# Performance work log

Measured on AMD Instinct MI355X. Metric: run time of the kernel, lower is better.

The kernel has to match this reference:

```python
import jax, jax.numpy as jnp
import numpy as np

WS = 7       # window size per spatial dim
SHIFT = 3    # cyclic shift = WS // 2
HEADS = 6


def _rel_pos_index():
    # [N, N] index into the (2*WS-1)^3 relative-position-bias table
    c = np.stack(np.meshgrid(np.arange(WS), np.arange(WS), np.arange(WS), indexing='ij')).reshape(3, -1)
    rel = (c[:, :, None] - c[:, None, :]).transpose(1, 2, 0) + (WS - 1)
    rel[:, :, 0] *= (2 * WS - 1) ** 2
    rel[:, :, 1] *= (2 * WS - 1)
    return rel.sum(-1)


def _attn_mask(D, H, W):
    # shifted-window attention mask: [nW, N, N] with 0 / -100
    img = np.zeros((D, H, W))
    sl = (slice(0, -WS), slice(-WS, -SHIFT), slice(-SHIFT, None))
    cnt = 0
    for d in sl:
        for h in sl:
            for w in sl:
                img[d, h, w] = cnt
                cnt += 1
    m = img.reshape(D // WS, WS, H // WS, WS, W // WS, WS).transpose(0, 2, 4, 1, 3, 5).reshape(-1, WS ** 3)
    return np.where(m[:, None, :] != m[:, :, None], -100.0, 0.0).astype(np.float32)


def _ln(x, g, b):
    mu = x.mean(-1, keepdims=True)
    var = ((x - mu) ** 2).mean(-1, keepdims=True)
    return (x - mu) * jax.lax.rsqrt(var + 1e-5) * g + b


def _win_part(x):
    B, D, H, W, C = x.shape
    x = x.reshape(B, D // WS, WS, H // WS, WS, W // WS, WS, C)
    return x.transpose(0, 1, 3, 5, 2, 4, 6, 7).reshape(B, -1, WS ** 3, C)


def _win_rev(xw, D, H, W):
    B, _, _, C = xw.shape
    x = xw.reshape(B, D // WS, H // WS, W // WS, WS, WS, WS, C)
    return x.transpose(0, 1, 4, 2, 5, 3, 6, 7).reshape(B, D, H, W, C)


def setup_inputs() -> dict:
    key = jax.random.key(0)
    ks = jax.random.split(key, 8)
    C, dff, Nh = 192, 768, HEADS
    s = 0.02
    return {
        'x': jax.random.normal(ks[0], (2, 28, 28, 28, C), jnp.float32),
        'ln1_g': jnp.ones((C,), jnp.float32),
        'ln1_b': jnp.zeros((C,), jnp.float32),
        'qkv_w': jax.random.normal(ks[1], (3 * C, C), jnp.float32) * s,
        'qkv_b': jnp.zeros((3 * C,), jnp.float32),
        'rpb': jax.random.normal(ks[2], ((2 * WS - 1) ** 3, Nh), jnp.float32) * s,
        'proj_w': jax.random.normal(ks[3], (C, C), jnp.float32) * s,
        'proj_b': jnp.zeros((C,), jnp.float32),
        'ln2_g': jnp.ones((C,), jnp.float32),
        'ln2_b': jnp.zeros((C,), jnp.float32),
        'fc1_w': jax.random.normal(ks[4], (dff, C), jnp.float32) * s,
        'fc1_b': jnp.zeros((dff,), jnp.float32),
        'fc2_w': jax.random.normal(ks[5], (C, dff), jnp.float32) * s,
        'fc2_b': jnp.zeros((C,), jnp.float32),
    }


def reference(x, ln1_g, ln1_b, qkv_w, qkv_b, rpb, proj_w, proj_b, ln2_g, ln2_b, fc1_w, fc1_b, fc2_w, fc2_b):
    B, D, H, W, C = x.shape
    hd = C // HEADS
    N = WS ** 3
    idx = jnp.asarray(_rel_pos_index())          # [N, N] int
    mask = jnp.asarray(_attn_mask(D, H, W))      # [nW, N, N]

    shortcut = x
    h = _ln(x, ln1_g, ln1_b)
    h = jnp.roll(h, (-SHIFT, -SHIFT, -SHIFT), axis=(1, 2, 3))
    xw = _win_part(h)                            # [B, nW, N, C]
    nW = xw.shape[1]

    qkv = xw @ qkv_w.T + qkv_b                   # [B, nW, N, 3C]
    qkv = qkv.reshape(B, nW, N, 3, HEADS, hd).transpose(3, 0, 1, 4, 2, 5)  # [3,B,nW,h,N,hd]
    q, k, v = qkv[0], qkv[1], qkv[2]

    scale = hd ** -0.5
    attn = jnp.einsum('bwhnd,bwhmd->bwhnm', q * scale, k)  # [B,nW,h,N,N]
    bias = rpb[idx].transpose(2, 0, 1)           # [h, N, N]
    attn = attn + bias + mask[None, :, None]
    attn = jax.nn.softmax(attn, axis=-1)

    o = jnp.einsum('bwhnm,bwhmd->bwhnd', attn, v)
    o = o.transpose(0, 1, 3, 2, 4).reshape(B, nW, N, C)
    o = o @ proj_w.T + proj_b
    o = _win_rev(o, D, H, W)
    o = jnp.roll(o, (SHIFT, SHIFT, SHIFT), axis=(1, 2, 3))

    x = shortcut + o
    h2 = _ln(x, ln2_g, ln2_b)
    h2 = jax.nn.gelu(h2 @ fc1_w.T + fc1_b, approximate=False)
    return x + (h2 @ fc2_w.T + fc2_b)
```

## Files before the change

### kernel.cpp

```cpp
#include <hip/hip_runtime.h>
#include <hip/hip_bf16.h>
#include <math.h>

typedef __hip_bfloat16 bf16;
typedef unsigned short u16;
typedef __attribute__((ext_vector_type(8))) short bf16x8;
typedef __attribute__((ext_vector_type(4))) float f32x4;
typedef __attribute__((ext_vector_type(16))) float f32x16;
typedef __attribute__((ext_vector_type(4))) unsigned u32x4;

__device__ __forceinline__ float us2f(u16 u) { return __uint_as_float(((unsigned)u) << 16); }
__device__ __forceinline__ u16 f2us(float f) { bf16 h = __float2bfloat16(f); return *(u16*)&h; }

__device__ __forceinline__ float wave_bcast_sum(float v) {
#pragma unroll
    for (int off = 32; off > 0; off >>= 1) v += __shfl_down(v, off);
    return __shfl(v, 0);
}

__device__ __forceinline__ void glds16(const u16* g, u16* l) {
    __builtin_amdgcn_global_load_lds((const __attribute__((address_space(1))) void*)g,
                                     (__attribute__((address_space(3))) void*)l, 16, 0, 0);
}

__global__ __launch_bounds__(256) void k_f2b(const float* __restrict__ in, u16* __restrict__ out, int n) {
    int i = blockIdx.x * 256 + threadIdx.x;
    if (i < n) out[i] = f2us(in[i]);
}

__global__ __launch_bounds__(256) void k_bias(const float* __restrict__ rpb, float* __restrict__ bt) {
    int idx = blockIdx.x * 256 + threadIdx.x;
    if (idx >= 6 * 352 * 352) return;
    int h = idx / (352 * 352);
    int r = idx - h * (352 * 352);
    int m = r / 352, n = r - m * 352;
    float v = 0.0f;
    if (m < 343 && n < 343) {
        int ni = n / 49, nr = n - ni * 49, nj = nr / 7, nk = nr - nj * 7;
        int mi = m / 49, mr = m - mi * 49, mj = mr / 7, mk = mr - mj * 7;
        int d = (ni - mi) * 169 + (nj - mj) * 13 + (nk - mk) + 1098;
        v = rpb[d * 6 + h] * 1.4426950408889634f;
    }
    bt[idx] = v;
}

__global__ __launch_bounds__(256) void k_ln1_winpart(
    const float* __restrict__ x, const float* __restrict__ g, const float* __restrict__ b,
    u16* __restrict__ out)
{
    int lane = threadIdx.x & 63;
    int t = blockIdx.x * 4 + (threadIdx.x >> 6);
    int bidx = t / (64 * 343);
    int r = t - bidx * (64 * 343);
    int w = r / 343;
    int n = r - w * 343;
    int wd = w >> 4, wh = (w >> 2) & 3, ww = w & 3;
    int i = n / 49, rem = n - i * 49;
    int j = rem / 7, k = rem - j * 7;
    int sd = wd * 7 + i + 3; if (sd >= 28) sd -= 28;
    int sh = wh * 7 + j + 3; if (sh >= 28) sh -= 28;
    int sw = ww * 7 + k + 3; if (sw >= 28) sw -= 28;
    size_t src = ((((size_t)bidx * 28 + sd) * 28 + sh) * 28 + sw) * 192;
    float v0 = x[src + lane], v1 = x[src + lane + 64], v2 = x[src + lane + 128];
    float s  = wave_bcast_sum(v0 + v1 + v2);
    float mu = s * (1.0f / 192.0f);
    float s2 = wave_bcast_sum(v0 * v0 + v1 * v1 + v2 * v2);
    float rs = rsqrtf(s2 * (1.0f / 192.0f) - mu * mu + 1e-5f);
    u16* op = out + (size_t)t * 192;
    op[lane]       = f2us((v0 - mu) * rs * g[lane]       + b[lane]);
    op[lane + 64]  = f2us((v1 - mu) * rs * g[lane + 64]  + b[lane + 64]);
    op[lane + 128] = f2us((v2 - mu) * rs * g[lane + 128] + b[lane + 128]);
}

__global__ __launch_bounds__(256) void k_add_winrev_ln2(
    const float* __restrict__ x, const u16* __restrict__ projw,
    const float* __restrict__ g, const float* __restrict__ b,
    float* __restrict__ x1, u16* __restrict__ h2)
{
    int lane = threadIdx.x & 63;
    int t = blockIdx.x * 4 + (threadIdx.x >> 6);
    int sw_ = t % 28, t1 = t / 28;
    int sh_ = t1 % 28, t2 = t1 / 28;
    int sd_ = t2 % 28, bidx = t2 / 28;
    int rd = sd_ + 25; if (rd >= 28) rd -= 28;
    int rh = sh_ + 25; if (rh >= 28) rh -= 28;
    int rw = sw_ + 25; if (rw >= 28) rw -= 28;
    int wd = rd / 7, i = rd - wd * 7;
    int wh = rh / 7, j = rh - wh * 7;
    int ww = rw / 7, k = rw - ww * 7;
    int w = (wd << 4) + (wh << 2) + ww;
    int n = (i * 7 + j) * 7 + k;
    size_t src = (((size_t)(bidx * 64 + w)) * 343 + n) * 192;
    const float* xp = x + (size_t)t * 192;
    float v0 = xp[lane]       + us2f(projw[src + lane]);
    float v1 = xp[lane + 64]  + us2f(projw[src + lane + 64]);
    float v2 = xp[lane + 128] + us2f(projw[src + lane + 128]);
    float* op = x1 + (size_t)t * 192;
    op[lane] = v0; op[lane + 64] = v1; op[lane + 128] = v2;
    float s  = wave_bcast_sum(v0 + v1 + v2);
    float mu = s * (1.0f / 192.0f);
    float s2 = wave_bcast_sum(v0 * v0 + v1 * v1 + v2 * v2);
    float rs = rsqrtf(s2 * (1.0f / 192.0f) - mu * mu + 1e-5f);
    u16* hp = h2 + (size_t)t * 192;
    hp[lane]       = f2us((v0 - mu) * rs * g[lane]       + b[lane]);
    hp[lane + 64]  = f2us((v1 - mu) * rs * g[lane + 64]  + b[lane + 64]);
    hp[lane + 128] = f2us((v2 - mu) * rs * g[lane + 128] + b[lane + 128]);
}

template<int ACT, int OUT>
__global__ __launch_bounds__(256) void k_gemm_mfma(
    const u16* __restrict__ A, const u16* __restrict__ W, const float* __restrict__ bias,
    u16* __restrict__ outB, float* __restrict__ outF, const float* __restrict__ resid,
    int M, int Nc, int K)
{
    __shared__ __align__(16) u16 As[2][128 * 32];
    __shared__ __align__(16) u16 Bs[2][64 * 32];
    int tid = threadIdx.x;
    int lane = tid & 63, wv = tid >> 6;
    int quad = lane >> 4, l16 = lane & 15;
    int m0 = blockIdx.y << 7, n0 = blockIdx.x << 6;

    f32x4 acc[2][4] = {};
    int rowA0 = tid >> 2;
    int rowA1 = rowA0 + 64;
    int koff = (tid & 3) << 3;

    const u16* gA0 = A + (size_t)(m0 + rowA0) * K + koff;
    const u16* gA1 = A + (size_t)(m0 + rowA1) * K + koff;
    const u16* gB0 = W + (size_t)(n0 + rowA0) * K + koff;

    int nt = K >> 5;
    glds16(gA0, &As[0][wv * 512]);
    glds16(gA1, &As[0][2048 + wv * 512]);
    glds16(gB0, &Bs[0][wv * 512]);
    asm volatile("s_waitcnt vmcnt(0)" ::: "memory");
    __builtin_amdgcn_s_barrier();

    int cur = 0;
    for (int t = 0; t < nt; ++t) {
        if (t + 1 < nt) {
            int k1 = (t + 1) << 5;
            glds16(gA0 + k1, &As[cur ^ 1][wv * 512]);
            glds16(gA1 + k1, &As[cur ^ 1][2048 + wv * 512]);
            glds16(gB0 + k1, &Bs[cur ^ 1][wv * 512]);
        }
        bf16x8 af[2], bfr[4];
#pragma unroll
        for (int mt = 0; mt < 2; mt++)
            af[mt] = *(const bf16x8*)&As[cur][(wv * 32 + mt * 16 + l16) * 32 + quad * 8];
#pragma unroll
        for (int nt2 = 0; nt2 < 4; nt2++)
            bfr[nt2] = *(const bf16x8*)&Bs[cur][(nt2 * 16 + l16) * 32 + quad * 8];
#pragma unroll
        for (int mt = 0; mt < 2; mt++)
#pragma unroll
            for (int nt2 = 0; nt2 < 4; nt2++)
                acc[mt][nt2] = __builtin_amdgcn_mfma_f32_16x16x32_bf16(af[mt], bfr[nt2], acc[mt][nt2], 0, 0, 0);
        asm volatile("s_waitcnt vmcnt(0)" ::: "memory");
        __builtin_amdgcn_s_barrier();
        cur ^= 1;
    }
#pragma unroll
    for (int mt = 0; mt < 2; mt++) {
#pragma unroll
        for (int nt2 = 0; nt2 < 4; nt2++) {
#pragma unroll
            for (int r = 0; r < 4; r++) {
                int m = m0 + wv * 32 + mt * 16 + quad * 4 + r;
                int n = n0 + nt2 * 16 + l16;
                float v = acc[mt][nt2][r] + bias[n];
                if (ACT == 1) v = 0.5f * v * (1.0f + erff(v * 0.70710678118654752f));
                size_t off = (size_t)m * Nc + n;
                if (OUT == 1) outB[off] = f2us(v);
                else outF[off] = resid[off] + v;
            }
        }
    }
}

__global__ __launch_bounds__(256) void k_attn(
    const u16* __restrict__ qkv, const float* __restrict__ biasT, u16* __restrict__ o_win)
{
    int head = blockIdx.x;
    int w = blockIdx.y;
    int bidx = blockIdx.z;
    __shared__ __align__(16) u16 Ks[352 * 40];
    __shared__ __align__(16) u16 Vt[32 * 360];
    __shared__ float invs[4][32];
    __shared__ unsigned char lab[352];
    int tid = threadIdx.x;
    int lane = tid & 63, wv = tid >> 6;
    int hi = lane >> 5, l31 = lane & 31;
    size_t base = ((size_t)(bidx * 64 + w)) * 343;

    for (int i = tid; i < 2816; i += 256) {
        int m = i >> 3;
        int d4 = (i & 7) << 2;
        ushort4 kv = {0, 0, 0, 0}, vv = {0, 0, 0, 0};
        if (m < 343) {
            size_t off = (base + m) * 576 + head * 32 + d4;
            kv = *(const ushort4*)(qkv + off + 192);
            vv = *(const ushort4*)(qkv + off + 384);
        }
        *(ushort4*)&Ks[m * 40 + d4] = kv;
        Vt[(d4 + 0) * 360 + m] = vv.x;
        Vt[(d4 + 1) * 360 + m] = vv.y;
        Vt[(d4 + 2) * 360 + m] = vv.z;
        Vt[(d4 + 3) * 360 + m] = vv.w;
    }
    int wd = w >> 4, wh = (w >> 2) & 3, ww = w & 3;
    for (int n = tid; n < 352; n += 256) {
        unsigned char lv = 255;
        if (n < 343) {
            int i = n / 49, rem = n - i * 49;
            int j = rem / 7, k = rem - j * 7;
            int gd = wd * 7 + i, gh = wh * 7 + j, gw = ww * 7 + k;
            int ld_ = (gd < 21) ? 0 : ((gd < 25) ? 1 : 2);
            int lh_ = (gh < 21) ? 0 : ((gh < 25) ? 1 : 2);
            int lw_ = (gw < 21) ? 0 : ((gw < 25) ? 1 : 2);
            lv = (unsigned char)(ld_ * 9 + lh_ * 3 + lw_);
        }
        lab[n] = lv;
    }
    __syncthreads();

    const float SL = 0.17677669529663687f * 1.4426950408889634f;
    const f32x16 z16 = {0,0,0,0,0,0,0,0,0,0,0,0,0,0,0,0};

    for (int tile = wv; tile < 11; tile += 4) {
        int n0 = tile * 32;
        int nq = n0 + l31; if (nq > 342) nq = 342;
        const u16* qp = qkv + (base + nq) * 576 + head * 32;
        bf16x8 bq0 = *(const bf16x8*)(qp + hi * 8);
        bf16x8 bq1 = *(const bf16x8*)(qp + 16 + hi * 8);
        unsigned lr = lab[n0 + l31];
        const float* bq = biasT + (size_t)head * 352 * 352 + n0 + l31;

        f32x16 o = z16;
        float psum = 0.0f;
        for (int c = 0; c < 11; ++c) {
            int mb = c * 32;
            const u16* kp = &Ks[(mb + l31) * 40 + hi * 8];
            bf16x8 ka0 = *(const bf16x8*)kp;
            bf16x8 ka1 = *(const bf16x8*)(kp + 16);
            f32x16 s = __builtin_amdgcn_mfma_f32_32x32x16_bf16(ka0, bq0, z16, 0, 0, 0);
            s = __builtin_amdgcn_mfma_f32_32x32x16_bf16(ka1, bq1, s, 0, 0, 0);
            unsigned labw[4];
#pragma unroll
            for (int g = 0; g < 4; ++g)
                labw[g] = *(const unsigned*)&lab[mb + hi * 4 + g * 8];
            float p[16];
#pragma unroll
            for (int r = 0; r < 16; ++r) {
                int g = r >> 2, q = r & 3;
                float bb = bq[(size_t)(mb + 4 * hi + 8 * g + q) * 352];
                float e = exp2f(fmaf(s[r], SL, bb));
                p[r] = (((labw[g] >> (8 * q)) & 255u) == lr) ? e : 0.0f;
                psum += p[r];
            }
            unsigned pk0 = (unsigned)f2us(p[0])  | ((unsigned)f2us(p[1])  << 16);
            unsigned pk1 = (unsigned)f2us(p[2])  | ((unsigned)f2us(p[3])  << 16);
            unsigned pk2 = (unsigned)f2us(p[4])  | ((unsigned)f2us(p[5])  << 16);
            unsigned pk3 = (unsigned)f2us(p[6])  | ((unsigned)f2us(p[7])  << 16);
            unsigned pk4 = (unsigned)f2us(p[8])  | ((unsigned)f2us(p[9])  << 16);
            unsigned pk5 = (unsigned)f2us(p[10]) | ((unsigned)f2us(p[11]) << 16);
            unsigned pk6 = (unsigned)f2us(p[12]) | ((unsigned)f2us(p[13]) << 16);
            unsigned pk7 = (unsigned)f2us(p[14]) | ((unsigned)f2us(p[15]) << 16);
            asm volatile("v_permlane32_swap_b32 %0, %1" : "+v"(pk0), "+v"(pk2));
            asm volatile("v_permlane32_swap_b32 %0, %1" : "+v"(pk1), "+v"(pk3));
            asm volatile("v_permlane32_swap_b32 %0, %1" : "+v"(pk4), "+v"(pk6));
            asm volatile("v_permlane32_swap_b32 %0, %1" : "+v"(pk5), "+v"(pk7));
            u32x4 A1 = {pk0, pk1, pk2, pk3};
            u32x4 A2 = {pk4, pk5, pk6, pk7};
            bf16x8 pa0 = __builtin_bit_cast(bf16x8, A1);
            bf16x8 pa1 = __builtin_bit_cast(bf16x8, A2);
            const u16* vp = &Vt[l31 * 360 + mb + hi * 8];
            bf16x8 vb0 = *(const bf16x8*)vp;
            bf16x8 vb1 = *(const bf16x8*)(vp + 16);
            o = __builtin_amdgcn_mfma_f32_32x32x16_bf16(pa0, vb0, o, 0, 0, 0);
            o = __builtin_amdgcn_mfma_f32_32x32x16_bf16(pa1, vb1, o, 0, 0, 0);
        }
        psum += __shfl_xor(psum, 32);
        float inv = 1.0f / psum;
        invs[wv][l31] = inv;
        asm volatile("s_waitcnt lgkmcnt(0)" ::: "memory");
        __builtin_amdgcn_sched_barrier(0);
#pragma unroll
        for (int r = 0; r < 16; ++r) {
            int crow = (r & 3) + 8 * (r >> 2) + 4 * hi;
            int n = n0 + crow;
            if (n < 343) {
                u16* op = o_win + (base + n) * 192 + head * 32;
                op[l31] = f2us(o[r] * invs[wv][crow]);
            }
        }
    }
}

extern "C" void kernel_launch(void* const* d_in, const int* in_sizes, int n_in,
                              void* d_out, int out_size, void* d_ws, size_t ws_size,
                              hipStream_t stream)
{
    const float* x      = (const float*)d_in[0];
    const float* ln1_g  = (const float*)d_in[1];
    const float* ln1_b  = (const float*)d_in[2];
    const float* qkv_w  = (const float*)d_in[3];
    const float* qkv_b  = (const float*)d_in[4];
    const float* rpb    = (const float*)d_in[5];
    const float* proj_w = (const float*)d_in[6];
    const float* proj_b = (const float*)d_in[7];
    const float* ln2_g  = (const float*)d_in[8];
    const float* ln2_b  = (const float*)d_in[9];
    const float* fc1_w  = (const float*)d_in[10];
    const float* fc1_b  = (const float*)d_in[11];
    const float* fc2_w  = (const float*)d_in[12];
    const float* fc2_b  = (const float*)d_in[13];

    const int M = 43904;
    const size_t MC  = (size_t)M * 192;
    const size_t MC2 = MC * 2;

    char* ws = (char*)d_ws;
    u16* hA     = (u16*)ws;
    u16* qkvb   = (u16*)(ws + MC2);
    u16* projw  = (u16*)(ws + MC2);
    u16* gbuf   = (u16*)(ws + MC2);
    u16* fc1_wb = (u16*)(ws + 51u * 1024 * 1024);
    u16* fc2_wb = (u16*)(ws + 51u * 1024 * 1024 + 294912);
    float* out  = (float*)d_out;
    u16* qkv_wb  = (u16*)d_out;
    u16* proj_wb = (u16*)d_out + 110592;
    float* biasT = (float*)((char*)d_out + 4u * 1024 * 1024);

    k_f2b<<<432, 256, 0, stream>>>(qkv_w, qkv_wb, 110592);
    k_f2b<<<144, 256, 0, stream>>>(proj_w, proj_wb, 36864);
    k_bias<<<2904, 256, 0, stream>>>(rpb, biasT);
    k_ln1_winpart<<<M / 4, 256, 0, stream>>>(x, ln1_g, ln1_b, hA);
    k_gemm_mfma<0, 1><<<dim3(9, 343), 256, 0, stream>>>(hA, qkv_wb, qkv_b, qkvb, nullptr, nullptr, M, 576, 192);
    k_attn<<<dim3(6, 64, 2), 256, 0, stream>>>(qkvb, biasT, hA);
    k_f2b<<<576, 256, 0, stream>>>(fc1_w, fc1_wb, 147456);
    k_f2b<<<576, 256, 0, stream>>>(fc2_w, fc2_wb, 147456);
    k_gemm_mfma<0, 1><<<dim3(3, 343), 256, 0, stream>>>(hA, proj_wb, proj_b, projw, nullptr, nullptr, M, 192, 192);
    k_add_winrev_ln2<<<M / 4, 256, 0, stream>>>(x, projw, ln2_g, ln2_b, out, hA);
    const int CH0 = 22016, CH1 = 21888;
    k_gemm_mfma<1, 1><<<dim3(12, 172), 256, 0, stream>>>(hA, fc1_wb, fc1_b, gbuf, nullptr, nullptr, CH0, 768, 192);
    k_gemm_mfma<0, 2><<<dim3(3, 172), 256, 0, stream>>>(gbuf, fc2_wb, fc2_b, nullptr, out, out, CH0, 192, 768);
    k_gemm_mfma<1, 1><<<dim3(12, 171), 256, 0, stream>>>(hA + (size_t)CH0 * 192, fc1_wb, fc1_b, gbuf, nullptr, nullptr, CH1, 768, 192);
    k_gemm_mfma<0, 2><<<dim3(3, 171), 256, 0, stream>>>(gbuf, fc2_wb, fc2_b, nullptr, out + (size_t)CH0 * 192, out + (size_t)CH0 * 192, CH1, 192, 768);
}
```

Before: 341.3 us.

## Widen GEMM K-tile with swizzled LDS, specialize unmasked attention windows, fuse prep kernels

The GEMM now stages 64-wide K tiles with an XOR-swizzled LDS layout, which halves the number of barrier iterations and is meant to reduce bank conflicts. In attention, the bias table is transposed so each lane reads it as contiguous float4 values that seed the MFMA accumulator. Windows that need no shift mask take a fast path that skips the label comparison. The small weight-conversion and bias-table kernels are merged into fewer launches. The larger LDS footprint may reduce GEMM occupancy.

```diff
diff --git a/kernel.cpp b/kernel.cpp
--- a/kernel.cpp
+++ b/kernel.cpp
@@ -23,25 +23,37 @@
                                      (__attribute__((address_space(3))) void*)l, 16, 0, 0);
 }
 
-__global__ __launch_bounds__(256) void k_f2b(const float* __restrict__ in, u16* __restrict__ out, int n) {
-    int i = blockIdx.x * 256 + threadIdx.x;
-    if (i < n) out[i] = f2us(in[i]);
-}
-
-__global__ __launch_bounds__(256) void k_bias(const float* __restrict__ rpb, float* __restrict__ bt) {
+__global__ __launch_bounds__(256) void k_prep(
+    const float* __restrict__ qkv_w, const float* __restrict__ proj_w,
+    const float* __restrict__ rpb,
+    u16* __restrict__ qkv_wb, u16* __restrict__ proj_wb, float* __restrict__ biasT)
+{
     int idx = blockIdx.x * 256 + threadIdx.x;
+    if (idx < 110592) { qkv_wb[idx] = f2us(qkv_w[idx]); return; }
+    idx -= 110592;
+    if (idx < 36864) { proj_wb[idx] = f2us(proj_w[idx]); return; }
+    idx -= 36864;
     if (idx >= 6 * 352 * 352) return;
     int h = idx / (352 * 352);
     int r = idx - h * (352 * 352);
-    int m = r / 352, n = r - m * 352;
+    int n = r / 352, m = r - n * 352;
     float v = 0.0f;
     if (m < 343 && n < 343) {
         int ni = n / 49, nr = n - ni * 49, nj = nr / 7, nk = nr - nj * 7;
         int mi = m / 49, mr = m - mi * 49, mj = mr / 7, mk = mr - mj * 7;
         int d = (ni - mi) * 169 + (nj - mj) * 13 + (nk - mk) + 1098;
-        v = rpb[d * 6 + h] * 1.4426950408889634f;
-    }
-    bt[idx] = v;
+        v = rpb[d * 6 + h] * 5.656854249492381f;
+    }
+    biasT[h * (352 * 352) + n * 352 + m] = v;
+}
+
+__global__ __launch_bounds__(256) void k_f2b2(
+    const float* __restrict__ fc1_w, const float* __restrict__ fc2_w,
+    u16* __restrict__ fc1_wb, u16* __restrict__ fc2_wb)
+{
+    int idx = blockIdx.x * 256 + threadIdx.x;
+    if (idx < 147456) fc1_wb[idx] = f2us(fc1_w[idx]);
+    else fc2_wb[idx - 147456] = f2us(fc2_w[idx - 147456]);
 }
 
 __global__ __launch_bounds__(256) void k_ln1_winpart(
@@ -113,62 +125,70 @@
     u16* __restrict__ outB, float* __restrict__ outF, const float* __restrict__ resid,
     int M, int Nc, int K)
 {
-    __shared__ __align__(16) u16 As[2][128 * 32];
-    __shared__ __align__(16) u16 Bs[2][64 * 32];
+    __shared__ __align__(16) u16 As[2][128 * 64];
+    __shared__ __align__(16) u16 Bs[2][64 * 64];
     int tid = threadIdx.x;
     int lane = tid & 63, wv = tid >> 6;
     int quad = lane >> 4, l16 = lane & 15;
     int m0 = blockIdx.y << 7, n0 = blockIdx.x << 6;
 
     f32x4 acc[2][4] = {};
-    int rowA0 = tid >> 2;
-    int rowA1 = rowA0 + 64;
-    int koff = (tid & 3) << 3;
-
-    const u16* gA0 = A + (size_t)(m0 + rowA0) * K + koff;
-    const u16* gA1 = A + (size_t)(m0 + rowA1) * K + koff;
-    const u16* gB0 = W + (size_t)(n0 + rowA0) * K + koff;
-
-    int nt = K >> 5;
-    glds16(gA0, &As[0][wv * 512]);
-    glds16(gA1, &As[0][2048 + wv * 512]);
-    glds16(gB0, &Bs[0][wv * 512]);
+
+    int srow = wv * 8 + (lane >> 3);
+    int swz  = ((lane & 7) << 3) ^ (((lane >> 3) & 7) << 3);
+    const u16* gA = A + (size_t)(m0 + srow) * K + swz;
+    const u16* gB = W + (size_t)(n0 + srow) * K + swz;
+    int rsA = 32 * K;
+
+    int nst = K >> 6;
+#define STAGE(buf, k0)                                                        \
+    {                                                                         \
+        _Pragma("unroll")                                                     \
+        for (int i = 0; i < 4; i++)                                           \
+            glds16(gA + (size_t)i * rsA + (k0), &As[buf][(i * 4 + wv) * 512]); \
+        _Pragma("unroll")                                                     \
+        for (int i = 0; i < 2; i++)                                           \
+            glds16(gB + (size_t)i * rsA + (k0), &Bs[buf][(i * 4 + wv) * 512]); \
+    }
+
+    STAGE(0, 0);
     asm volatile("s_waitcnt vmcnt(0)" ::: "memory");
     __builtin_amdgcn_s_barrier();
 
+    int rswz = (l16 & 7) << 3;
     int cur = 0;
-    for (int t = 0; t < nt; ++t) {
-        if (t + 1 < nt) {
-            int k1 = (t + 1) << 5;
-            glds16(gA0 + k1, &As[cur ^ 1][wv * 512]);
-            glds16(gA1 + k1, &As[cur ^ 1][2048 + wv * 512]);
-            glds16(gB0 + k1, &Bs[cur ^ 1][wv * 512]);
-        }
-        bf16x8 af[2], bfr[4];
-#pragma unroll
-        for (int mt = 0; mt < 2; mt++)
-            af[mt] = *(const bf16x8*)&As[cur][(wv * 32 + mt * 16 + l16) * 32 + quad * 8];
-#pragma unroll
-        for (int nt2 = 0; nt2 < 4; nt2++)
-            bfr[nt2] = *(const bf16x8*)&Bs[cur][(nt2 * 16 + l16) * 32 + quad * 8];
-#pragma unroll
-        for (int mt = 0; mt < 2; mt++)
-#pragma unroll
-            for (int nt2 = 0; nt2 < 4; nt2++)
-                acc[mt][nt2] = __builtin_amdgcn_mfma_f32_16x16x32_bf16(af[mt], bfr[nt2], acc[mt][nt2], 0, 0, 0);
+    for (int t = 0; t < nst; ++t) {
+        if (t + 1 < nst) STAGE(cur ^ 1, (t + 1) << 6);
+#pragma unroll
+        for (int kk = 0; kk < 2; kk++) {
+            int ko = (kk * 32 + quad * 8) ^ rswz;
+            bf16x8 af[2], bfr[4];
+#pragma unroll
+            for (int mt = 0; mt < 2; mt++)
+                af[mt] = *(const bf16x8*)&As[cur][(wv * 32 + mt * 16 + l16) * 64 + ko];
+#pragma unroll
+            for (int nt = 0; nt < 4; nt++)
+                bfr[nt] = *(const bf16x8*)&Bs[cur][(nt * 16 + l16) * 64 + ko];
+#pragma unroll
+            for (int mt = 0; mt < 2; mt++)
+#pragma unroll
+                for (int nt = 0; nt < 4; nt++)
+                    acc[mt][nt] = __builtin_amdgcn_mfma_f32_16x16x32_bf16(af[mt], bfr[nt], acc[mt][nt], 0, 0, 0);
+        }
         asm volatile("s_waitcnt vmcnt(0)" ::: "memory");
         __builtin_amdgcn_s_barrier();
         cur ^= 1;
     }
+#undef STAGE
 #pragma unroll
     for (int mt = 0; mt < 2; mt++) {
 #pragma unroll
-        for (int nt2 = 0; nt2 < 4; nt2++) {
+        for (int nt = 0; nt < 4; nt++) {
 #pragma unroll
             for (int r = 0; r < 4; r++) {
                 int m = m0 + wv * 32 + mt * 16 + quad * 4 + r;
-                int n = n0 + nt2 * 16 + l16;
-                float v = acc[mt][nt2][r] + bias[n];
+                int n = n0 + nt * 16 + l16;
+                float v = acc[mt][nt][r] + bias[n];
                 if (ACT == 1) v = 0.5f * v * (1.0f + erff(v * 0.70710678118654752f));
                 size_t off = (size_t)m * Nc + n;
                 if (OUT == 1) outB[off] = f2us(v);
@@ -209,6 +229,7 @@
         Vt[(d4 + 3) * 360 + m] = vv.w;
     }
     int wd = w >> 4, wh = (w >> 2) & 3, ww = w & 3;
+    bool uni = (wd < 3) && (wh < 3) && (ww < 3);
     for (int n = tid; n < 352; n += 256) {
         unsigned char lv = 255;
         if (n < 343) {
@@ -234,30 +255,48 @@
         bf16x8 bq0 = *(const bf16x8*)(qp + hi * 8);
         bf16x8 bq1 = *(const bf16x8*)(qp + 16 + hi * 8);
         unsigned lr = lab[n0 + l31];
-        const float* bq = biasT + (size_t)head * 352 * 352 + n0 + l31;
+        const float* bq = biasT + ((size_t)head * 352 + (n0 + l31)) * 352;
 
         f32x16 o = z16;
         float psum = 0.0f;
-        for (int c = 0; c < 11; ++c) {
-            int mb = c * 32;
+
+        auto chunk = [&](int mb, int mode) {
             const u16* kp = &Ks[(mb + l31) * 40 + hi * 8];
             bf16x8 ka0 = *(const bf16x8*)kp;
             bf16x8 ka1 = *(const bf16x8*)(kp + 16);
-            f32x16 s = __builtin_amdgcn_mfma_f32_32x32x16_bf16(ka0, bq0, z16, 0, 0, 0);
+            f32x16 s;
+#pragma unroll
+            for (int g = 0; g < 4; ++g) {
+                float4 bb = *(const float4*)(bq + mb + hi * 4 + g * 8);
+                s[4 * g + 0] = bb.x; s[4 * g + 1] = bb.y;
+                s[4 * g + 2] = bb.z; s[4 * g + 3] = bb.w;
+            }
+            s = __builtin_amdgcn_mfma_f32_32x32x16_bf16(ka0, bq0, s, 0, 0, 0);
             s = __builtin_amdgcn_mfma_f32_32x32x16_bf16(ka1, bq1, s, 0, 0, 0);
-            unsigned labw[4];
-#pragma unroll
-            for (int g = 0; g < 4; ++g)
-                labw[g] = *(const unsigned*)&lab[mb + hi * 4 + g * 8];
             float p[16];
-#pragma unroll
-            for (int r = 0; r < 16; ++r) {
-                int g = r >> 2, q = r & 3;
-                float bb = bq[(size_t)(mb + 4 * hi + 8 * g + q) * 352];
-                float e = exp2f(fmaf(s[r], SL, bb));
-                p[r] = (((labw[g] >> (8 * q)) & 255u) == lr) ? e : 0.0f;
-                psum += p[r];
+            if (mode == 0) {
+#pragma unroll
+                for (int r = 0; r < 16; ++r) p[r] = exp2f(s[r] * SL);
+            } else if (mode == 1) {
+#pragma unroll
+                for (int r = 0; r < 16; ++r) {
+                    int m = mb + 4 * hi + 8 * (r >> 2) + (r & 3);
+                    float e = exp2f(s[r] * SL);
+                    p[r] = (m < 343) ? e : 0.0f;
+                }
+            } else {
+                unsigned labw[4];
+#pragma unroll
+                for (int g = 0; g < 4; ++g)
+                    labw[g] = *(const unsigned*)&lab[mb + hi * 4 + g * 8];
+#pragma unroll
+                for (int r = 0; r < 16; ++r) {
+                    float e = exp2f(s[r] * SL);
+                    p[r] = (((labw[r >> 2] >> (8 * (r & 3))) & 255u) == lr) ? e : 0.0f;
+                }
             }
+#pragma unroll
+            for (int r = 0; r < 16; ++r) psum += p[r];
             unsigned pk0 = (unsigned)f2us(p[0])  | ((unsigned)f2us(p[1])  << 16);
             unsigned pk1 = (unsigned)f2us(p[2])  | ((unsigned)f2us(p[3])  << 16);
             unsigned pk2 = (unsigned)f2us(p[4])  | ((unsigned)f2us(p[5])  << 16);
@@ -279,7 +318,15 @@
             bf16x8 vb1 = *(const bf16x8*)(vp + 16);
             o = __builtin_amdgcn_mfma_f32_32x32x16_bf16(pa0, vb0, o, 0, 0, 0);
             o = __builtin_amdgcn_mfma_f32_32x32x16_bf16(pa1, vb1, o, 0, 0, 0);
-        }
+        };
+
+        if (uni) {
+            for (int c = 0; c < 10; ++c) chunk(c * 32, 0);
+            chunk(320, 1);
+        } else {
+            for (int c = 0; c < 11; ++c) chunk(c * 32, 2);
+        }
+
         psum += __shfl_xor(psum, 32);
         float inv = 1.0f / psum;
         invs[wv][l31] = inv;
@@ -332,14 +379,11 @@
     u16* proj_wb = (u16*)d_out + 110592;
     float* biasT = (float*)((char*)d_out + 4u * 1024 * 1024);
 
-    k_f2b<<<432, 256, 0, stream>>>(qkv_w, qkv_wb, 110592);
-    k_f2b<<<144, 256, 0, stream>>>(proj_w, proj_wb, 36864);
-    k_bias<<<2904, 256, 0, stream>>>(rpb, biasT);
+    k_prep<<<3481, 256, 0, stream>>>(qkv_w, proj_w, rpb, qkv_wb, proj_wb, biasT);
     k_ln1_winpart<<<M / 4, 256, 0, stream>>>(x, ln1_g, ln1_b, hA);
     k_gemm_mfma<0, 1><<<dim3(9, 343), 256, 0, stream>>>(hA, qkv_wb, qkv_b, qkvb, nullptr, nullptr, M, 576, 192);
     k_attn<<<dim3(6, 64, 2), 256, 0, stream>>>(qkvb, biasT, hA);
-    k_f2b<<<576, 256, 0, stream>>>(fc1_w, fc1_wb, 147456);
-    k_f2b<<<576, 256, 0, stream>>>(fc2_w, fc2_wb, 147456);
+    k_f2b2<<<1152, 256, 0, stream>>>(fc1_w, fc2_w, fc1_wb, fc2_wb);
     k_gemm_mfma<0, 1><<<dim3(3, 343), 256, 0, stream>>>(hA, proj_wb, proj_b, projw, nullptr, nullptr, M, 192, 192);
     k_add_winrev_ln2<<<M / 4, 256, 0, stream>>>(x, projw, ln2_g, ln2_b, out, hA);
     const int CH0 = 22016, CH1 = 21888;
```

New measurement: 344.7 us. About the same (+1.0%).
